# Performance work log

Measured on AMD Instinct MI355X. Metric: run time of the kernel, lower is better.

## Reference

```python
import jax, jax.numpy as jnp
import numpy as np

B, T, M, D, H, DH = 2, 2048, 2048, 384, 4, 96
NM, DF, R, NA = 8, 1536, 16, 4
S = 0.02  # weight init scale

PARAM_NAMES = ['cWq','cbq','cWk','cbk','cWv','cbv','cWo','cbo',
               'sWq','sbq','sWk','sbk','sWv','sbv','sWo','sbo',
               'gW','gb','f1W','f1b','f2W','f2b','adA','adB',
               'ln1g','ln1b','ln2g','ln2b','ln3g','ln3b']

def setup_inputs() -> dict:
    key = jax.random.key(0)
    ks = jax.random.split(key, 20)
    n = lambda k, sh, s=1.0: jax.random.normal(k, sh, dtype=jnp.float32) * s
    z = lambda sh: jnp.zeros(sh, dtype=jnp.float32)
    o = lambda sh: jnp.ones(sh, dtype=jnp.float32)
    return {
        'x': n(ks[0], (B, T, D)),
        'mem': n(ks[1], (B, M, D)),
        'motif_ctrl': n(ks[2], (B, NM)),
        'adapter_idx': 1,
        'cWq': n(ks[3], (D, D), S), 'cbq': z((D,)),
        'cWk': n(ks[4], (D, D), S), 'cbk': z((D,)),
        'cWv': n(ks[5], (D, D), S), 'cbv': z((D,)),
        'cWo': n(ks[6], (D, D), S), 'cbo': z((D,)),
        'sWq': n(ks[7], (D, D), S), 'sbq': z((D,)),
        'sWk': n(ks[8], (D, D), S), 'sbk': z((D,)),
        'sWv': n(ks[9], (D, D), S), 'sbv': z((D,)),
        'sWo': n(ks[10], (D, D), S), 'sbo': z((D,)),
        'gW': n(ks[11], (H, NM), S), 'gb': z((H,)),
        'f1W': n(ks[12], (DF, D), S), 'f1b': z((DF,)),
        'f2W': n(ks[13], (D, DF), S), 'f2b': z((D,)),
        'adA': n(ks[14], (NA, R, D), S),
        'adB': n(ks[15], (NA, D, R), S),
        'ln1g': o((D,)), 'ln1b': z((D,)),
        'ln2g': o((D,)), 'ln2b': z((D,)),
        'ln3g': o((D,)), 'ln3b': z((D,)),
    }

def _lin(x, W, b):
    return x @ W.T + b  # torch nn.Linear convention: W is [out, in]

def _layernorm(x, g, b):
    mu = x.mean(-1, keepdims=True)
    var = ((x - mu) ** 2).mean(-1, keepdims=True)
    return (x - mu) * jax.lax.rsqrt(var + 1e-5) * g + b

def _block(x, mem, motif_ctrl, adapter_idx, p):
    scale = 1.0 / np.sqrt(DH).astype(np.float32)
    # --- cross-attention over memory ---
    h = _layernorm(x, p['ln1g'], p['ln1b'])
    q = _lin(h, p['cWq'], p['cbq']).reshape(B, T, H, DH)
    k = _lin(mem, p['cWk'], p['cbk']).reshape(B, M, H, DH)
    v = _lin(mem, p['cWv'], p['cbv']).reshape(B, M, H, DH)
    A = jax.nn.softmax(jnp.einsum('bthd,bmhd->bhtm', q, k) * scale, axis=-1)
    z = jnp.einsum('bhtm,bmhd->bthd', A, v).reshape(B, T, D)
    x = x + _lin(z, p['cWo'], p['cbo'])
    # --- motif-gated self-attention (post-softmax per-head gate) ---
    h = _layernorm(x, p['ln2g'], p['ln2b'])
    gates = jax.nn.sigmoid(motif_ctrl @ p['gW'].T + p['gb'])  # [B, H]
    q = _lin(h, p['sWq'], p['sbq']).reshape(B, T, H, DH)
    k = _lin(h, p['sWk'], p['sbk']).reshape(B, T, H, DH)
    v = _lin(h, p['sWv'], p['sbv']).reshape(B, T, H, DH)
    A = jax.nn.softmax(jnp.einsum('bthd,bshd->bhts', q, k) * scale, axis=-1)
    A = A * gates[:, :, None, None]
    z = jnp.einsum('bhts,bshd->bthd', A, v).reshape(B, T, D)
    x = x + _lin(z, p['sWo'], p['sbo'])
    # --- LoRA-adapter FFN ---
    h = _layernorm(x, p['ln3g'], p['ln3b'])
    f = _lin(jax.nn.gelu(_lin(h, p['f1W'], p['f1b']), approximate=False), p['f2W'], p['f2b'])
    f = f + (h @ p['adA'][adapter_idx].T) @ p['adB'][adapter_idx].T
    return x + f

def reference(x, mem, motif_ctrl, adapter_idx,
              cWq, cbq, cWk, cbk, cWv, cbv, cWo, cbo,
              sWq, sbq, sWk, sbk, sWv, sbv, sWo, sbo,
              gW, gb, f1W, f1b, f2W, f2b, adA, adB,
              ln1g, ln1b, ln2g, ln2b, ln3g, ln3b):
    p = dict(zip(PARAM_NAMES, (cWq, cbq, cWk, cbk, cWv, cbv, cWo, cbo,
                               sWq, sbq, sWk, sbk, sWv, sbv, sWo, sbo,
                               gW, gb, f1W, f1b, f2W, f2b, adA, adB,
                               ln1g, ln1b, ln2g, ln2b, ln3g, ln3b)))
    return _block(x, mem, motif_ctrl, int(adapter_idx), p)
```

## Files before the change

### kernel.cpp

```cpp
#include <hip/hip_runtime.h>
#include <hip/hip_bf16.h>
#include <math.h>

#define B_   2
#define T_   2048
#define M_   2048
#define D_   384
#define H_   4
#define DH_  96
#define NM_  8
#define DF_  1536
#define R_   16
#define NR_  4096

typedef unsigned short u16;
typedef u16    u16x8  __attribute__((ext_vector_type(8)));
typedef u16    u16x4  __attribute__((ext_vector_type(4)));
typedef __bf16 bf16x8 __attribute__((ext_vector_type(8)));
typedef float  f32x4  __attribute__((ext_vector_type(4)));

union V8 { u16x8 u; bf16x8 b; };
__device__ __forceinline__ bf16x8 as_bf(u16x8 x) { V8 v; v.u = x; return v.b; }

__device__ __forceinline__ u16 f2bf(float f) {
    unsigned u = __float_as_uint(f);
    unsigned r = (u + 0x7fffu + ((u >> 16) & 1u)) >> 16;
    return (u16)r;
}
__device__ __forceinline__ float bf2f(u16 u) {
    return __uint_as_float(((unsigned)u) << 16);
}

__device__ __forceinline__ void load16(const u16* g, u16* l) {
    __builtin_amdgcn_global_load_lds(
        (const __attribute__((address_space(1))) void*)g,
        (__attribute__((address_space(3))) void*)l, 16, 0, 0);
}

__global__ __launch_bounds__(256)
void setup_kernel(const float* cWq, const float* cWk, const float* cWv, const float* cWo,
                  const float* sWq, const float* sWk, const float* sWv, const float* sWo,
                  const float* f1W, const float* f2W, const float* adA, const float* adB,
                  const float* mem,
                  u16* Wqkv_c, u16* Wco, u16* Wqkv_s, u16* Wso,
                  u16* Wf1, u16* Wf2, u16* WadA, u16* WadB, u16* memb,
                  const float* cbq, const float* cbk, const float* cbv,
                  const float* sbq, const float* sbk, const float* sbv,
                  float* bqkv_c, float* bqkv_s,
                  const float* mc, const float* gW, const float* gb, float* gates) {
    int seg = blockIdx.y;
    if (seg == 13) {
        for (int i = blockIdx.x * 256 + threadIdx.x; i < 2312; i += gridDim.x * 256) {
            if (i < 1152) {
                bqkv_c[i] = (i < 384) ? cbq[i] : (i < 768 ? cbk[i - 384] : cbv[i - 768]);
            } else if (i < 2304) {
                int j = i - 1152;
                bqkv_s[j] = (j < 384) ? sbq[j] : (j < 768 ? sbk[j - 384] : sbv[j - 768]);
            } else {
                int k = i - 2304;
                int b = k / H_, h = k % H_;
                float s = gb[h];
                for (int n = 0; n < NM_; n++)
                    s += mc[b * NM_ + n] * gW[h * NM_ + n];
                gates[k] = 1.f / (1.f + __expf(-s));
            }
        }
        return;
    }
    const float* s; u16* d; int n;
    switch (seg) {
        case 0:  s = cWq; d = Wqkv_c;           n = 147456; break;
        case 1:  s = cWk; d = Wqkv_c + 147456;  n = 147456; break;
        case 2:  s = cWv; d = Wqkv_c + 294912;  n = 147456; break;
        case 3:  s = cWo; d = Wco;              n = 147456; break;
        case 4:  s = sWq; d = Wqkv_s;           n = 147456; break;
        case 5:  s = sWk; d = Wqkv_s + 147456;  n = 147456; break;
        case 6:  s = sWv; d = Wqkv_s + 294912;  n = 147456; break;
        case 7:  s = sWo; d = Wso;              n = 147456; break;
        case 8:  s = f1W; d = Wf1;              n = 589824; break;
        case 9:  s = f2W; d = Wf2;              n = 589824; break;
        case 10: s = adA; d = WadA;             n = 24576;  break;
        case 11: s = adB; d = WadB;             n = 24576;  break;
        default: s = mem; d = memb;             n = 1572864; break;
    }
    for (int i = blockIdx.x * 256 + threadIdx.x; i < n; i += gridDim.x * 256)
        d[i] = f2bf(s[i]);
}

__global__ __launch_bounds__(384)
void ln_kernel(const float* __restrict__ x, const float* __restrict__ g,
               const float* __restrict__ b, u16* __restrict__ out) {
    __shared__ float sm[8];
    int row = blockIdx.x;
    int t = threadIdx.x;
    float v = x[(long)row * D_ + t];

    float s = v;
    for (int o = 32; o > 0; o >>= 1) s += __shfl_down(s, o);
    if ((t & 63) == 0) sm[t >> 6] = s;
    __syncthreads();
    float mu = 0.f;
    for (int i = 0; i < 6; i++) mu += sm[i];
    mu *= (1.f / D_);
    __syncthreads();

    float d = v - mu;
    s = d * d;
    for (int o = 32; o > 0; o >>= 1) s += __shfl_down(s, o);
    if ((t & 63) == 0) sm[t >> 6] = s;
    __syncthreads();
    float var = 0.f;
    for (int i = 0; i < 6; i++) var += sm[i];
    var *= (1.f / D_);

    float r = rsqrtf(var + 1e-5f);
    out[(long)row * D_ + t] = f2bf(d * r * g[t] + b[t]);
}

template<int MT, int ACT, bool OBF, bool VT, bool LORA, bool LORAA>
__global__ __launch_bounds__(256)
void gemm_uni(const u16* __restrict__ A0, const u16* __restrict__ A1, int aswitch,
              const u16* __restrict__ W, const float* __restrict__ bias,
              const float* __restrict__ res, void* __restrict__ Cout, int NC, int K,
              u16* __restrict__ Vt, int vtbase,
              const u16* __restrict__ Tl, const u16* __restrict__ adW,
              u16* __restrict__ TlOut, const int* __restrict__ aidx) {
    constexpr int NREG = 4 * MT + 8;
    constexpr int HALF = NREG * 512;
    __shared__ __align__(16) u16 S[2 * HALF];
    int tid = threadIdx.x, w = tid >> 6, lane = tid & 63;
    int l15 = lane & 15, quad = lane >> 4;
    int bm = blockIdx.y * (MT * 32), bn = blockIdx.x * 64;
    bool loraBlk = LORAA && (bn >= NC);

    const u16* Ap = (bn < aswitch) ? A0 : A1;
    const u16* Wb = W;
    if (LORAA && loraBlk) Wb = adW + (long)aidx[0] * 6144;

    const u16* GP[MT + 2];
    int LO[MT + 2];
    #pragma unroll
    for (int i = 0; i < MT + 2; i++) {
        int r = i * 4 + w;
        const u16* src;
        if (r < 4 * MT) {
            int mt = r >> 1, kc = r & 1;
            src = Ap + (long)(bm + mt * 16 + l15) * K + kc * 32 + quad * 8;
        } else {
            int rw = r - 4 * MT, nt = rw >> 1, kc = rw & 1;
            if (LORAA && loraBlk)
                src = Wb + (long)((nt * 16 + l15) & 15) * K + kc * 32 + quad * 8;
            else
                src = Wb + (long)(bn + nt * 16 + l15) * K + kc * 32 + quad * 8;
        }
        GP[i] = src;
        LO[i] = r * 512;
    }

    f32x4 acc[MT][2];
    #pragma unroll
    for (int s = 0; s < MT; s++)
        #pragma unroll
        for (int j = 0; j < 2; j++) acc[s][j] = (f32x4){0.f, 0.f, 0.f, 0.f};

    int niter = K >> 6;
    #pragma unroll
    for (int i = 0; i < MT + 2; i++) load16(GP[i], S + LO[i]);

    for (int it = 0; it < niter; it++) {
        __syncthreads();
        int cur = (it & 1) * HALF, nxt = HALF - cur;
        if (it + 1 < niter) {
            int k = (it + 1) << 6;
            #pragma unroll
            for (int i = 0; i < MT + 2; i++) load16(GP[i] + k, S + nxt + LO[i]);
        }
        #pragma unroll
        for (int kc = 0; kc < 2; kc++) {
            u16x8 af[MT], bfv[2];
            #pragma unroll
            for (int s = 0; s < MT; s++)
                af[s] = *(const u16x8*)(S + cur + (((w & 1) * MT + s) * 2 + kc) * 512 + lane * 8);
            #pragma unroll
            for (int j = 0; j < 2; j++)
                bfv[j] = *(const u16x8*)(S + cur + (4 * MT + (((w >> 1) * 2 + j) * 2 + kc)) * 512 + lane * 8);
            #pragma unroll
            for (int s = 0; s < MT; s++)
                #pragma unroll
                for (int j = 0; j < 2; j++)
                    acc[s][j] = __builtin_amdgcn_mfma_f32_16x16x32_bf16(
                        as_bf(af[s]), as_bf(bfv[j]), acc[s][j], 0, 0, 0);
        }
    }

    if (LORA) {
        long ao = (long)aidx[0] * 6144;
        u16x8 tlf[MT], adf[2];
        #pragma unroll
        for (int s = 0; s < MT; s++) {
            #pragma unroll
            for (int e = 0; e < 8; e++) tlf[s][e] = 0;
            if (quad < 2)
                tlf[s] = *(const u16x8*)(Tl + (long)(bm + ((w & 1) * MT + s) * 16 + l15) * 16 + quad * 8);
        }
        #pragma unroll
        for (int j = 0; j < 2; j++) {
            #pragma unroll
            for (int e = 0; e < 8; e++) adf[j][e] = 0;
            if (quad < 2)
                adf[j] = *(const u16x8*)(adW + ao + (long)(bn + ((w >> 1) * 2 + j) * 16 + l15) * 16 + quad * 8);
        }
        #pragma unroll
        for (int s = 0; s < MT; s++)
            #pragma unroll
            for (int j = 0; j < 2; j++)
                acc[s][j] = __builtin_amdgcn_mfma_f32_16x16x32_bf16(
                    as_bf(tlf[s]), as_bf(adf[j]), acc[s][j], 0, 0, 0);
    }

    #pragma unroll
    for (int mi = 0; mi < MT; mi++) {
        int mt = (w & 1) * MT + mi;
        int rowb = bm + mt * 16 + quad * 4;
        #pragma unroll
        for (int nj = 0; nj < 2; nj++) {
            int coll = ((w >> 1) * 2 + nj) * 16 + l15;
            int col = bn + coll;
            if (LORAA && loraBlk) {
                if (coll < 16) {
                    #pragma unroll
                    for (int r = 0; r < 4; r++)
                        TlOut[(long)(rowb + r) * 16 + coll] = f2bf(acc[mi][nj][r]);
                }
            } else {
                float bv = bias ? bias[col] : 0.f;
                if (VT && col >= vtbase) {
                    int vc = col - vtbase;
                    int b = rowb >> 11, rowl = rowb & 2047;
                    u16x4 ov;
                    #pragma unroll
                    for (int r = 0; r < 4; r++) ov[r] = f2bf(acc[mi][nj][r] + bv);
                    *(u16x4*)(Vt + ((long)b * 384 + vc) * 2048 + rowl) = ov;
                } else {
                    #pragma unroll
                    for (int r = 0; r < 4; r++) {
                        float v = acc[mi][nj][r] + bv;
                        if (ACT == 1) v = 0.5f * v * (1.f + erff(v * 0.70710678118654752f));
                        long idx = (long)(rowb + r) * NC + col;
                        if (res) v += res[idx];
                        if (OBF) ((u16*)Cout)[idx] = f2bf(v);
                        else     ((float*)Cout)[idx] = v;
                    }
                }
            }
        }
    }
}

__global__ __launch_bounds__(256)
void attn_mfma(const u16* __restrict__ Qg, int qs,
               const u16* __restrict__ Kg, int ks,
               const u16* __restrict__ Vt,
               u16* __restrict__ Po, float* __restrict__ Pl) {
    __shared__ __align__(16) u16 Ks[2][6144];
    __shared__ __align__(16) u16 Vs[2][6144];
    __shared__ __align__(16) u16 Ps[4][2][1088];
    const float SCALE = 0.10206207261596575f;

    int tid = threadIdx.x, wv = tid >> 6, lane = tid & 63;
    int l15 = lane & 15, quad = lane >> 4;
    int bh = blockIdx.y, b = bh >> 2, h = bh & 3;
    int split = blockIdx.z;
    int q0 = blockIdx.x * 128 + wv * 32;

    const u16* Qb = Qg + (long)(b * 2048 + q0) * qs + h * 96;
    const u16* Kb = Kg + (long)(b * 2048 + split * 512) * ks + h * 96;
    const u16* Vb = Vt + (long)(b * 384 + h * 96) * 2048 + split * 512;

    u16x8 qf[2][3];
    #pragma unroll
    for (int g = 0; g < 2; g++)
        #pragma unroll
        for (int t = 0; t < 3; t++)
            qf[g][t] = *(const u16x8*)(Qb + (long)(g * 16 + l15) * qs + t * 32 + quad * 8);

    f32x4 o[2][6];
    #pragma unroll
    for (int g = 0; g < 2; g++)
        #pragma unroll
        for (int i = 0; i < 6; i++) o[g][i] = (f32x4){0.f, 0.f, 0.f, 0.f};
    float rs[2][4] = {{0.f, 0.f, 0.f, 0.f}, {0.f, 0.f, 0.f, 0.f}};

    const u16* KgI[3]; int KlO[3]; const u16* VgI[3]; int VlO[3];
    #pragma unroll
    for (int i = 0; i < 3; i++) {
        int r = i * 4 + wv;
        int ksub = r & 3, kst = r >> 2;
        KgI[i] = Kb + (long)(ksub * 16 + l15) * ks + kst * 32 + quad * 8;
        KlO[i] = (ksub * 3 + kst) * 512;
        int nt = r >> 1, t2 = r & 1;
        VgI[i] = Vb + (long)(nt * 16 + l15) * 2048 + t2 * 32 + quad * 8;
        VlO[i] = r * 512;
    }

    #pragma unroll
    for (int i = 0; i < 3; i++) {
        load16(KgI[i], &Ks[0][0] + KlO[i]);
        load16(VgI[i], &Vs[0][0] + VlO[i]);
    }

    for (int it = 0; it < 8; it++) {
        __syncthreads();
        int cur = it & 1, nxt = cur ^ 1;
        if (it + 1 < 8) {
            int j = (it + 1) * 64;
            #pragma unroll
            for (int i = 0; i < 3; i++) {
                load16(KgI[i] + (long)j * ks, &Ks[nxt][0] + KlO[i]);
                load16(VgI[i] + j, &Vs[nxt][0] + VlO[i]);
            }
        }

        f32x4 sc[2][4];
        #pragma unroll
        for (int g = 0; g < 2; g++)
            #pragma unroll
            for (int s = 0; s < 4; s++) sc[g][s] = (f32x4){0.f, 0.f, 0.f, 0.f};
        #pragma unroll
        for (int s = 0; s < 4; s++)
            #pragma unroll
            for (int t = 0; t < 3; t++) {
                u16x8 kf = *(const u16x8*)(&Ks[cur][0] + (s * 3 + t) * 512 + lane * 8);
                sc[0][s] = __builtin_amdgcn_mfma_f32_16x16x32_bf16(as_bf(qf[0][t]), as_bf(kf), sc[0][s], 0, 0, 0);
                sc[1][s] = __builtin_amdgcn_mfma_f32_16x16x32_bf16(as_bf(qf[1][t]), as_bf(kf), sc[1][s], 0, 0, 0);
            }

        #pragma unroll
        for (int g = 0; g < 2; g++)
            #pragma unroll
            for (int s = 0; s < 4; s++) {
                int base = (s >> 1) * 544 + ((((s & 1) << 1) | (l15 >> 3))) * 136 + (l15 & 7);
                #pragma unroll
                for (int r = 0; r < 4; r++) {
                    float p = __expf(sc[g][s][r] * SCALE);
                    rs[g][r] += p;
                    Ps[wv][g][base + (quad * 4 + r) * 8] = f2bf(p);
                }
            }

        #pragma unroll
        for (int t2 = 0; t2 < 2; t2++) {
            u16x8 pf0 = *(const u16x8*)(&Ps[wv][0][0] + t2 * 544 + quad * 136 + l15 * 8);
            u16x8 pf1 = *(const u16x8*)(&Ps[wv][1][0] + t2 * 544 + quad * 136 + l15 * 8);
            #pragma unroll
            for (int nt = 0; nt < 6; nt++) {
                u16x8 vf = *(const u16x8*)(&Vs[cur][0] + (nt * 2 + t2) * 512 + lane * 8);
                o[0][nt] = __builtin_amdgcn_mfma_f32_16x16x32_bf16(as_bf(pf0), as_bf(vf), o[0][nt], 0, 0, 0);
                o[1][nt] = __builtin_amdgcn_mfma_f32_16x16x32_bf16(as_bf(pf1), as_bf(vf), o[1][nt], 0, 0, 0);
            }
        }
    }

    #pragma unroll
    for (int off = 1; off < 16; off <<= 1)
        #pragma unroll
        for (int g = 0; g < 2; g++)
            #pragma unroll
            for (int r = 0; r < 4; r++) rs[g][r] += __shfl_xor(rs[g][r], off);

    #pragma unroll
    for (int g = 0; g < 2; g++) {
        u16* Pob = Po + ((long)(split * 8 + bh) * 2048 + q0 + g * 16) * 96;
        #pragma unroll
        for (int nt = 0; nt < 6; nt++)
            #pragma unroll
            for (int r = 0; r < 4; r++)
                Pob[(long)(quad * 4 + r) * 96 + nt * 16 + l15] = f2bf(o[g][nt][r]);
        if (l15 == 0) {
            long mb = (long)(split * 8 + bh) * 2048 + q0 + g * 16 + quad * 4;
            #pragma unroll
            for (int r = 0; r < 4; r++) Pl[mb + r] = rs[g][r];
        }
    }
}

__global__ __launch_bounds__(256)
void attn_combine(const u16* __restrict__ Po, const float* __restrict__ Pl,
                  const float* __restrict__ gates, u16* __restrict__ Z) {
    int bh = blockIdx.y, b = bh >> 2, h = bh & 3;
    int tid = threadIdx.x;
    int rl = tid >> 2, part = tid & 3;
    int row = blockIdx.x * 64 + rl;
    long rbase = (long)bh * 2048 + row;

    float L = 0.f;
    #pragma unroll
    for (int s = 0; s < 4; s++) L += Pl[s * 16384 + rbase];
    float g = gates ? gates[bh] : 1.f;
    float sc = g / L;

    u16* Zr = Z + ((long)(b * 2048) + row) * 384 + h * 96 + part * 24;
    #pragma unroll
    for (int i = 0; i < 24; i += 4) {
        f32x4 acc = (f32x4){0.f, 0.f, 0.f, 0.f};
        #pragma unroll
        for (int s = 0; s < 4; s++) {
            u16x4 v = *(const u16x4*)(Po + ((long)s * 16384 + rbase) * 96 + part * 24 + i);
            #pragma unroll
            for (int e = 0; e < 4; e++) acc[e] += bf2f(v[e]);
        }
        u16x4 ov;
        #pragma unroll
        for (int e = 0; e < 4; e++) ov[e] = f2bf(acc[e] * sc);
        *(u16x4*)(Zr + i) = ov;
    }
}

extern "C" void kernel_launch(void* const* d_in, const int* in_sizes, int n_in,
                              void* d_out, int out_size, void* d_ws, size_t ws_size,
                              hipStream_t stream) {
    const float* x    = (const float*)d_in[0];
    const float* mem  = (const float*)d_in[1];
    const float* mc   = (const float*)d_in[2];
    const int*   aidx = (const int*)d_in[3];
    const float* cWq = (const float*)d_in[4],  *cbq = (const float*)d_in[5];
    const float* cWk = (const float*)d_in[6],  *cbk = (const float*)d_in[7];
    const float* cWv = (const float*)d_in[8],  *cbv = (const float*)d_in[9];
    const float* cWo = (const float*)d_in[10], *cbo = (const float*)d_in[11];
    const float* sWq = (const float*)d_in[12], *sbq = (const float*)d_in[13];
    const float* sWk = (const float*)d_in[14], *sbk = (const float*)d_in[15];
    const float* sWv = (const float*)d_in[16], *sbv = (const float*)d_in[17];
    const float* sWo = (const float*)d_in[18], *sbo = (const float*)d_in[19];
    const float* gW  = (const float*)d_in[20], *gb  = (const float*)d_in[21];
    const float* f1W = (const float*)d_in[22], *f1b = (const float*)d_in[23];
    const float* f2W = (const float*)d_in[24], *f2b = (const float*)d_in[25];
    const float* adA = (const float*)d_in[26], *adB = (const float*)d_in[27];
    const float* ln1g = (const float*)d_in[28], *ln1b = (const float*)d_in[29];
    const float* ln2g = (const float*)d_in[30], *ln2b = (const float*)d_in[31];
    const float* ln3g = (const float*)d_in[32], *ln3b = (const float*)d_in[33];

    u16* p = (u16*)d_ws;
    u16* H      = p; p += (size_t)NR_ * 384;
    u16* bufQKV = p; p += (size_t)NR_ * 1152;
    u16* Vt     = p; p += (size_t)B_ * 384 * 2048;
    u16* Zb     = p; p += (size_t)NR_ * 384;
    u16* F      = p; p += (size_t)NR_ * 1536;
    u16* Tl     = p; p += (size_t)NR_ * 16;
    u16* memb   = p; p += (size_t)NR_ * 384;
    u16* Wqkv_c = p; p += 442368;
    u16* Wco    = p; p += 147456;
    u16* Wqkv_s = p; p += 442368;
    u16* Wso    = p; p += 147456;
    u16* Wf1    = p; p += 589824;
    u16* Wf2    = p; p += 589824;
    u16* WadA   = p; p += 24576;
    u16* WadB   = p; p += 24576;
    u16* Po     = p; p += (size_t)4 * 8 * 2048 * 96;
    p += ((size_t)p & 1);
    float* fp = (float*)(((size_t)p + 3) & ~(size_t)3);
    float* X1 = fp;     fp += (size_t)NR_ * 384;
    float* X2 = fp;     fp += (size_t)NR_ * 384;
    float* Pl = fp;     fp += (size_t)4 * 8 * 2048;
    float* bqkv_c = fp; fp += 1152;
    float* bqkv_s = fp; fp += 1152;
    float* gbuf   = fp; fp += 8;

    setup_kernel<<<dim3(96, 14), 256, 0, stream>>>(
        cWq, cWk, cWv, cWo, sWq, sWk, sWv, sWo, f1W, f2W, adA, adB, mem,
        Wqkv_c, Wco, Wqkv_s, Wso, Wf1, Wf2, WadA, WadB, memb,
        cbq, cbk, cbv, sbq, sbk, sbv, bqkv_c, bqkv_s, mc, gW, gb, gbuf);

    const float* nf = nullptr;
    const u16* nu = nullptr;
    ln_kernel<<<NR_, 384, 0, stream>>>(x, ln1g, ln1b, H);
    gemm_uni<2, 0, true, true, false, false><<<dim3(18, 64), 256, 0, stream>>>(
        H, memb, 384, Wqkv_c, bqkv_c, nf, bufQKV, 1152, 384, Vt, 768, nu, nu, nullptr, nullptr);
    attn_mfma<<<dim3(16, 8, 4), 256, 0, stream>>>(bufQKV, 1152, bufQKV + 384, 1152, Vt, Po, Pl);
    attn_combine<<<dim3(32, 8), 256, 0, stream>>>(Po, Pl, nullptr, Zb);
    gemm_uni<1, 0, false, false, false, false><<<dim3(6, 128), 256, 0, stream>>>(
        Zb, Zb, 0, Wco, cbo, x, X1, 384, 384, nullptr, 0, nu, nu, nullptr, nullptr);

    ln_kernel<<<NR_, 384, 0, stream>>>(X1, ln2g, ln2b, H);
    gemm_uni<2, 0, true, true, false, false><<<dim3(18, 64), 256, 0, stream>>>(
        H, H, 0, Wqkv_s, bqkv_s, nf, bufQKV, 1152, 384, Vt, 768, nu, nu, nullptr, nullptr);
    attn_mfma<<<dim3(16, 8, 4), 256, 0, stream>>>(bufQKV, 1152, bufQKV + 384, 1152, Vt, Po, Pl);
    attn_combine<<<dim3(32, 8), 256, 0, stream>>>(Po, Pl, gbuf, Zb);
    gemm_uni<1, 0, false, false, false, false><<<dim3(6, 128), 256, 0, stream>>>(
        Zb, Zb, 0, Wso, sbo, X1, X2, 384, 384, nullptr, 0, nu, nu, nullptr, nullptr);

    ln_kernel<<<NR_, 384, 0, stream>>>(X2, ln3g, ln3b, H);
    gemm_uni<2, 1, true, false, false, true><<<dim3(25, 64), 256, 0, stream>>>(
        H, H, 0, Wf1, f1b, nf, F, 1536, 384, nullptr, 0, nu, WadA, Tl, aidx);
    gemm_uni<1, 0, false, false, true, false><<<dim3(6, 128), 256, 0, stream>>>(
        F, F, 0, Wf2, f2b, X2, d_out, 384, 1536, nullptr, 0, Tl, WadB, nullptr, aidx);
}
```

Baseline: 355.1 us.

## Double attention KV split count and shrink LDS footprint with single-buffered V

Raises the key-dimension split of the attention kernel from 4 to 8, so each block covers 256 keys in 4 iterations and the grid doubles to 1024 blocks. V is now single-buffered and loaded in the same iteration it is consumed, with an extra barrier before the PV MFMAs. The P scratch padding is removed. This cuts LDS use, which may allow more resident blocks and better occupancy. In exchange, the V load is no longer overlapped with compute, the combine kernel reads twice as many partials, and the unpadded P layout may cause LDS bank conflicts.

```diff
diff --git a/kernel.cpp b/kernel.cpp
--- a/kernel.cpp
+++ b/kernel.cpp
@@ -12,6 +12,7 @@
 #define DF_  1536
 #define R_   16
 #define NR_  4096
+#define SPL  8
 
 typedef unsigned short u16;
 typedef u16    u16x8  __attribute__((ext_vector_type(8)));
@@ -263,8 +264,8 @@
                const u16* __restrict__ Vt,
                u16* __restrict__ Po, float* __restrict__ Pl) {
     __shared__ __align__(16) u16 Ks[2][6144];
-    __shared__ __align__(16) u16 Vs[2][6144];
-    __shared__ __align__(16) u16 Ps[4][2][1088];
+    __shared__ __align__(16) u16 Vs[6144];
+    __shared__ __align__(16) u16 Ps[4][2][1024];
     const float SCALE = 0.10206207261596575f;
 
     int tid = threadIdx.x, wv = tid >> 6, lane = tid & 63;
@@ -274,8 +275,8 @@
     int q0 = blockIdx.x * 128 + wv * 32;
 
     const u16* Qb = Qg + (long)(b * 2048 + q0) * qs + h * 96;
-    const u16* Kb = Kg + (long)(b * 2048 + split * 512) * ks + h * 96;
-    const u16* Vb = Vt + (long)(b * 384 + h * 96) * 2048 + split * 512;
+    const u16* Kb = Kg + (long)(b * 2048 + split * 256) * ks + h * 96;
+    const u16* Vb = Vt + (long)(b * 384 + h * 96) * 2048 + split * 256;
 
     u16x8 qf[2][3];
     #pragma unroll
@@ -291,7 +292,7 @@
         for (int i = 0; i < 6; i++) o[g][i] = (f32x4){0.f, 0.f, 0.f, 0.f};
     float rs[2][4] = {{0.f, 0.f, 0.f, 0.f}, {0.f, 0.f, 0.f, 0.f}};
 
-    const u16* KgI[3]; int KlO[3]; const u16* VgI[3]; int VlO[3];
+    const u16* KgI[3]; int KlO[3]; const u16* VgI[3]; u16* VlP[3];
     #pragma unroll
     for (int i = 0; i < 3; i++) {
         int r = i * 4 + wv;
@@ -300,25 +301,22 @@
         KlO[i] = (ksub * 3 + kst) * 512;
         int nt = r >> 1, t2 = r & 1;
         VgI[i] = Vb + (long)(nt * 16 + l15) * 2048 + t2 * 32 + quad * 8;
-        VlO[i] = r * 512;
-    }
-
-    #pragma unroll
-    for (int i = 0; i < 3; i++) {
-        load16(KgI[i], &Ks[0][0] + KlO[i]);
-        load16(VgI[i], &Vs[0][0] + VlO[i]);
-    }
-
-    for (int it = 0; it < 8; it++) {
+        VlP[i] = &Vs[0] + r * 512;
+    }
+
+    #pragma unroll
+    for (int i = 0; i < 3; i++) load16(KgI[i], &Ks[0][0] + KlO[i]);
+
+    for (int it = 0; it < 4; it++) {
+        int cur = it & 1, nxt = cur ^ 1;
         __syncthreads();
-        int cur = it & 1, nxt = cur ^ 1;
-        if (it + 1 < 8) {
-            int j = (it + 1) * 64;
-            #pragma unroll
-            for (int i = 0; i < 3; i++) {
-                load16(KgI[i] + (long)j * ks, &Ks[nxt][0] + KlO[i]);
-                load16(VgI[i] + j, &Vs[nxt][0] + VlO[i]);
-            }
+        int j = it * 64;
+        #pragma unroll
+        for (int i = 0; i < 3; i++) load16(VgI[i] + j, VlP[i]);
+        if (it + 1 < 4) {
+            int jn = (it + 1) * 64;
+            #pragma unroll
+            for (int i = 0; i < 3; i++) load16(KgI[i] + (long)jn * ks, &Ks[nxt][0] + KlO[i]);
         }
 
         f32x4 sc[2][4];
@@ -339,7 +337,7 @@
         for (int g = 0; g < 2; g++)
             #pragma unroll
             for (int s = 0; s < 4; s++) {
-                int base = (s >> 1) * 544 + ((((s & 1) << 1) | (l15 >> 3))) * 136 + (l15 & 7);
+                int base = (s >> 1) * 512 + ((((s & 1) << 1) | (l15 >> 3))) * 128 + (l15 & 7);
                 #pragma unroll
                 for (int r = 0; r < 4; r++) {
                     float p = __expf(sc[g][s][r] * SCALE);
@@ -348,13 +346,14 @@
                 }
             }
 
+        __syncthreads();
         #pragma unroll
         for (int t2 = 0; t2 < 2; t2++) {
-            u16x8 pf0 = *(const u16x8*)(&Ps[wv][0][0] + t2 * 544 + quad * 136 + l15 * 8);
-            u16x8 pf1 = *(const u16x8*)(&Ps[wv][1][0] + t2 * 544 + quad * 136 + l15 * 8);
+            u16x8 pf0 = *(const u16x8*)(&Ps[wv][0][0] + t2 * 512 + quad * 128 + l15 * 8);
+            u16x8 pf1 = *(const u16x8*)(&Ps[wv][1][0] + t2 * 512 + quad * 128 + l15 * 8);
             #pragma unroll
             for (int nt = 0; nt < 6; nt++) {
-                u16x8 vf = *(const u16x8*)(&Vs[cur][0] + (nt * 2 + t2) * 512 + lane * 8);
+                u16x8 vf = *(const u16x8*)(&Vs[0] + (nt * 2 + t2) * 512 + lane * 8);
                 o[0][nt] = __builtin_amdgcn_mfma_f32_16x16x32_bf16(as_bf(pf0), as_bf(vf), o[0][nt], 0, 0, 0);
                 o[1][nt] = __builtin_amdgcn_mfma_f32_16x16x32_bf16(as_bf(pf1), as_bf(vf), o[1][nt], 0, 0, 0);
             }
@@ -395,7 +394,7 @@
 
     float L = 0.f;
     #pragma unroll
-    for (int s = 0; s < 4; s++) L += Pl[s * 16384 + rbase];
+    for (int s = 0; s < SPL; s++) L += Pl[s * 16384 + rbase];
     float g = gates ? gates[bh] : 1.f;
     float sc = g / L;
 
@@ -404,7 +403,7 @@
     for (int i = 0; i < 24; i += 4) {
         f32x4 acc = (f32x4){0.f, 0.f, 0.f, 0.f};
         #pragma unroll
-        for (int s = 0; s < 4; s++) {
+        for (int s = 0; s < SPL; s++) {
             u16x4 v = *(const u16x4*)(Po + ((long)s * 16384 + rbase) * 96 + part * 24 + i);
             #pragma unroll
             for (int e = 0; e < 4; e++) acc[e] += bf2f(v[e]);
@@ -455,12 +454,11 @@
     u16* Wf2    = p; p += 589824;
     u16* WadA   = p; p += 24576;
     u16* WadB   = p; p += 24576;
-    u16* Po     = p; p += (size_t)4 * 8 * 2048 * 96;
-    p += ((size_t)p & 1);
+    u16* Po     = p; p += (size_t)SPL * 8 * 2048 * 96;
     float* fp = (float*)(((size_t)p + 3) & ~(size_t)3);
     float* X1 = fp;     fp += (size_t)NR_ * 384;
     float* X2 = fp;     fp += (size_t)NR_ * 384;
-    float* Pl = fp;     fp += (size_t)4 * 8 * 2048;
+    float* Pl = fp;     fp += (size_t)SPL * 8 * 2048;
     float* bqkv_c = fp; fp += 1152;
     float* bqkv_s = fp; fp += 1152;
     float* gbuf   = fp; fp += 8;
@@ -475,7 +473,7 @@
     ln_kernel<<<NR_, 384, 0, stream>>>(x, ln1g, ln1b, H);
     gemm_uni<2, 0, true, true, false, false><<<dim3(18, 64), 256, 0, stream>>>(
         H, memb, 384, Wqkv_c, bqkv_c, nf, bufQKV, 1152, 384, Vt, 768, nu, nu, nullptr, nullptr);
-    attn_mfma<<<dim3(16, 8, 4), 256, 0, stream>>>(bufQKV, 1152, bufQKV + 384, 1152, Vt, Po, Pl);
+    attn_mfma<<<dim3(16, 8, SPL), 256, 0, stream>>>(bufQKV, 1152, bufQKV + 384, 1152, Vt, Po, Pl);
     attn_combine<<<dim3(32, 8), 256, 0, stream>>>(Po, Pl, nullptr, Zb);
     gemm_uni<1, 0, false, false, false, false><<<dim3(6, 128), 256, 0, stream>>>(
         Zb, Zb, 0, Wco, cbo, x, X1, 384, 384, nullptr, 0, nu, nu, nullptr, nullptr);
@@ -483,7 +481,7 @@
     ln_kernel<<<NR_, 384, 0, stream>>>(X1, ln2g, ln2b, H);
     gemm_uni<2, 0, true, true, false, false><<<dim3(18, 64), 256, 0, stream>>>(
         H, H, 0, Wqkv_s, bqkv_s, nf, bufQKV, 1152, 384, Vt, 768, nu, nu, nullptr, nullptr);
-    attn_mfma<<<dim3(16, 8, 4), 256, 0, stream>>>(bufQKV, 1152, bufQKV + 384, 1152, Vt, Po, Pl);
+    attn_mfma<<<dim3(16, 8, SPL), 256, 0, stream>>>(bufQKV, 1152, bufQKV + 384, 1152, Vt, Po, Pl);
     attn_combine<<<dim3(32, 8), 256, 0, stream>>>(Po, Pl, gbuf, Zb);
     gemm_uni<1, 0, false, false, false, false><<<dim3(6, 128), 256, 0, stream>>>(
         Zb, Zb, 0, Wso, sbo, X1, X2, 384, 384, nullptr, 0, nu, nu, nullptr, nullptr);
```

After: 363.4 us. 1.02x slower.

## Fuse LayerNorm into QKV/FFN GEMM prologue and attention combine into output-projection GEMM

Applied to the files above, without the earlier changes.

Removes the standalone LayerNorm and attention-combine kernels. LayerNorm statistics are now computed per 64-row tile inside the following GEMM, which normalizes fp32 rows to bf16 while staging the A tile into shared memory. The split-K attention partials are summed and scaled inside the output-projection GEMM prologue. This saves launches and the intermediate H/Z round trips through global memory, at the cost of recomputing LN statistics in every N-block, register-path A loads instead of async copies, and a one-pass variance formula.

```diff
diff --git a/kernel.cpp b/kernel.cpp
--- a/kernel.cpp
+++ b/kernel.cpp
@@ -12,6 +12,7 @@
 #define DF_  1536
 #define R_   16
 #define NR_  4096
+#define SPL  4
 
 typedef unsigned short u16;
 typedef u16    u16x8  __attribute__((ext_vector_type(8)));
@@ -87,105 +88,129 @@
         d[i] = f2bf(s[i]);
 }
 
-__global__ __launch_bounds__(384)
-void ln_kernel(const float* __restrict__ x, const float* __restrict__ g,
-               const float* __restrict__ b, u16* __restrict__ out) {
-    __shared__ float sm[8];
-    int row = blockIdx.x;
-    int t = threadIdx.x;
-    float v = x[(long)row * D_ + t];
-
-    float s = v;
-    for (int o = 32; o > 0; o >>= 1) s += __shfl_down(s, o);
-    if ((t & 63) == 0) sm[t >> 6] = s;
-    __syncthreads();
-    float mu = 0.f;
-    for (int i = 0; i < 6; i++) mu += sm[i];
-    mu *= (1.f / D_);
-    __syncthreads();
-
-    float d = v - mu;
-    s = d * d;
-    for (int o = 32; o > 0; o >>= 1) s += __shfl_down(s, o);
-    if ((t & 63) == 0) sm[t >> 6] = s;
-    __syncthreads();
-    float var = 0.f;
-    for (int i = 0; i < 6; i++) var += sm[i];
-    var *= (1.f / D_);
-
-    float r = rsqrtf(var + 1e-5f);
-    out[(long)row * D_ + t] = f2bf(d * r * g[t] + b[t]);
-}
-
-template<int MT, int ACT, bool OBF, bool VT, bool LORA, bool LORAA>
+template<int ACT, bool OBF, bool VT, bool LORAA>
 __global__ __launch_bounds__(256)
-void gemm_uni(const u16* __restrict__ A0, const u16* __restrict__ A1, int aswitch,
-              const u16* __restrict__ W, const float* __restrict__ bias,
-              const float* __restrict__ res, void* __restrict__ Cout, int NC, int K,
-              u16* __restrict__ Vt, int vtbase,
-              const u16* __restrict__ Tl, const u16* __restrict__ adW,
-              u16* __restrict__ TlOut, const int* __restrict__ aidx) {
-    constexpr int NREG = 4 * MT + 8;
-    constexpr int HALF = NREG * 512;
-    __shared__ __align__(16) u16 S[2 * HALF];
+void gemm_ln(const float* __restrict__ Xf, const u16* __restrict__ A1, int aswitch,
+             const float* __restrict__ lng, const float* __restrict__ lnb,
+             const u16* __restrict__ W, const float* __restrict__ bias,
+             void* __restrict__ Cout, int NC,
+             u16* __restrict__ Vt, int vtbase,
+             const u16* __restrict__ adW, u16* __restrict__ TlOut,
+             const int* __restrict__ aidx) {
+    const int K = 384;
+    __shared__ __align__(16) u16 SA[2][4096];
+    __shared__ __align__(16) u16 SW[2][4096];
+    __shared__ float smu[64], sr[64];
+    __shared__ float slg[384], slb[384];
     int tid = threadIdx.x, w = tid >> 6, lane = tid & 63;
     int l15 = lane & 15, quad = lane >> 4;
-    int bm = blockIdx.y * (MT * 32), bn = blockIdx.x * 64;
+    int bm = blockIdx.y * 64, bn = blockIdx.x * 64;
     bool loraBlk = LORAA && (bn >= NC);
-
-    const u16* Ap = (bn < aswitch) ? A0 : A1;
+    bool pass = (bn >= aswitch);
+
     const u16* Wb = W;
     if (LORAA && loraBlk) Wb = adW + (long)aidx[0] * 6144;
 
-    const u16* GP[MT + 2];
-    int LO[MT + 2];
-    #pragma unroll
-    for (int i = 0; i < MT + 2; i++) {
-        int r = i * 4 + w;
-        const u16* src;
-        if (r < 4 * MT) {
-            int mt = r >> 1, kc = r & 1;
-            src = Ap + (long)(bm + mt * 16 + l15) * K + kc * 32 + quad * 8;
-        } else {
-            int rw = r - 4 * MT, nt = rw >> 1, kc = rw & 1;
-            if (LORAA && loraBlk)
-                src = Wb + (long)((nt * 16 + l15) & 15) * K + kc * 32 + quad * 8;
-            else
-                src = Wb + (long)(bn + nt * 16 + l15) * K + kc * 32 + quad * 8;
-        }
-        GP[i] = src;
-        LO[i] = r * 512;
-    }
-
-    f32x4 acc[MT][2];
-    #pragma unroll
-    for (int s = 0; s < MT; s++)
+    const u16* WG[2]; int WO[2];
+    #pragma unroll
+    for (int i = 0; i < 2; i++) {
+        int r = i * 4 + w, nt = r >> 1, kc = r & 1;
+        int wrow = (LORAA && loraBlk) ? ((nt * 16 + l15) & 15) : (bn + nt * 16 + l15);
+        WG[i] = Wb + (long)wrow * K + kc * 32 + quad * 8;
+        WO[i] = r * 512;
+    }
+
+    if (!pass) {
+        int row = tid >> 2, q4 = tid & 3;
+        const float* src = Xf + (long)(bm + row) * K + q4 * 96;
+        float s = 0.f, s2 = 0.f;
+        #pragma unroll
+        for (int i = 0; i < 24; i++) {
+            f32x4 v = *(const f32x4*)(src + i * 4);
+            #pragma unroll
+            for (int e = 0; e < 4; e++) { s += v[e]; s2 += v[e] * v[e]; }
+        }
+        s  += __shfl_xor(s, 1);  s  += __shfl_xor(s, 2);
+        s2 += __shfl_xor(s2, 1); s2 += __shfl_xor(s2, 2);
+        if (q4 == 0) {
+            float mu = s * (1.f / 384.f);
+            float var = s2 * (1.f / 384.f) - mu * mu;
+            smu[row] = mu;
+            sr[row] = rsqrtf(var + 1e-5f);
+        }
+        if (tid < 192) {
+            f32x4 g4 = *(const f32x4*)(lng + tid * 2);
+            slg[tid * 2] = g4[0]; slg[tid * 2 + 1] = g4[1];
+            f32x4 b4 = *(const f32x4*)(lnb + tid * 2);
+            slb[tid * 2] = b4[0]; slb[tid * 2 + 1] = b4[1];
+        }
+    }
+    #pragma unroll
+    for (int i = 0; i < 2; i++) load16(WG[i], &SW[0][0] + WO[i]);
+    __syncthreads();
+
+    {
+        int row = tid & 63;
+        #pragma unroll
+        for (int i = 0; i < 2; i++) {
+            int kg = (tid >> 6) + i * 4;
+            int k = kg * 8;
+            u16x8 hv;
+            if (pass) {
+                hv = *(const u16x8*)(A1 + (long)(bm + row) * K + k);
+            } else {
+                const float* src = Xf + (long)(bm + row) * K + k;
+                float mu = smu[row], r = sr[row];
+                #pragma unroll
+                for (int e = 0; e < 8; e++)
+                    hv[e] = f2bf((src[e] - mu) * r * slg[k + e] + slb[k + e]);
+            }
+            *(u16x8*)(&SA[0][0] + ((row >> 4) * 2 + (kg >> 2)) * 512 + (kg & 3) * 128 + (row & 15) * 8) = hv;
+        }
+    }
+
+    f32x4 acc[2][2];
+    #pragma unroll
+    for (int s = 0; s < 2; s++)
         #pragma unroll
         for (int j = 0; j < 2; j++) acc[s][j] = (f32x4){0.f, 0.f, 0.f, 0.f};
 
-    int niter = K >> 6;
-    #pragma unroll
-    for (int i = 0; i < MT + 2; i++) load16(GP[i], S + LO[i]);
-
-    for (int it = 0; it < niter; it++) {
+    for (int it = 0; it < 6; it++) {
         __syncthreads();
-        int cur = (it & 1) * HALF, nxt = HALF - cur;
-        if (it + 1 < niter) {
-            int k = (it + 1) << 6;
-            #pragma unroll
-            for (int i = 0; i < MT + 2; i++) load16(GP[i] + k, S + nxt + LO[i]);
+        int cur = it & 1, nxt = cur ^ 1;
+        if (it + 1 < 6) {
+            int k0 = (it + 1) * 64;
+            #pragma unroll
+            for (int i = 0; i < 2; i++) load16(WG[i] + k0, &SW[nxt][0] + WO[i]);
+            int row = tid & 63;
+            #pragma unroll
+            for (int i = 0; i < 2; i++) {
+                int kg = (tid >> 6) + i * 4;
+                int k = k0 + kg * 8;
+                u16x8 hv;
+                if (pass) {
+                    hv = *(const u16x8*)(A1 + (long)(bm + row) * K + k);
+                } else {
+                    const float* src = Xf + (long)(bm + row) * K + k;
+                    float mu = smu[row], r = sr[row];
+                    #pragma unroll
+                    for (int e = 0; e < 8; e++)
+                        hv[e] = f2bf((src[e] - mu) * r * slg[k + e] + slb[k + e]);
+                }
+                *(u16x8*)(&SA[nxt][0] + ((row >> 4) * 2 + (kg >> 2)) * 512 + (kg & 3) * 128 + (row & 15) * 8) = hv;
+            }
         }
         #pragma unroll
         for (int kc = 0; kc < 2; kc++) {
-            u16x8 af[MT], bfv[2];
-            #pragma unroll
-            for (int s = 0; s < MT; s++)
-                af[s] = *(const u16x8*)(S + cur + (((w & 1) * MT + s) * 2 + kc) * 512 + lane * 8);
+            u16x8 af[2], bfv[2];
+            #pragma unroll
+            for (int s = 0; s < 2; s++)
+                af[s] = *(const u16x8*)(&SA[cur][0] + (((w & 1) * 2 + s) * 2 + kc) * 512 + lane * 8);
             #pragma unroll
             for (int j = 0; j < 2; j++)
-                bfv[j] = *(const u16x8*)(S + cur + (4 * MT + (((w >> 1) * 2 + j) * 2 + kc)) * 512 + lane * 8);
-            #pragma unroll
-            for (int s = 0; s < MT; s++)
+                bfv[j] = *(const u16x8*)(&SW[cur][0] + ((((w >> 1) * 2 + j)) * 2 + kc) * 512 + lane * 8);
+            #pragma unroll
+            for (int s = 0; s < 2; s++)
                 #pragma unroll
                 for (int j = 0; j < 2; j++)
                     acc[s][j] = __builtin_amdgcn_mfma_f32_16x16x32_bf16(
@@ -193,35 +218,9 @@
         }
     }
 
-    if (LORA) {
-        long ao = (long)aidx[0] * 6144;
-        u16x8 tlf[MT], adf[2];
-        #pragma unroll
-        for (int s = 0; s < MT; s++) {
-            #pragma unroll
-            for (int e = 0; e < 8; e++) tlf[s][e] = 0;
-            if (quad < 2)
-                tlf[s] = *(const u16x8*)(Tl + (long)(bm + ((w & 1) * MT + s) * 16 + l15) * 16 + quad * 8);
-        }
-        #pragma unroll
-        for (int j = 0; j < 2; j++) {
-            #pragma unroll
-            for (int e = 0; e < 8; e++) adf[j][e] = 0;
-            if (quad < 2)
-                adf[j] = *(const u16x8*)(adW + ao + (long)(bn + ((w >> 1) * 2 + j) * 16 + l15) * 16 + quad * 8);
-        }
-        #pragma unroll
-        for (int s = 0; s < MT; s++)
-            #pragma unroll
-            for (int j = 0; j < 2; j++)
-                acc[s][j] = __builtin_amdgcn_mfma_f32_16x16x32_bf16(
-                    as_bf(tlf[s]), as_bf(adf[j]), acc[s][j], 0, 0, 0);
-    }
-
-    #pragma unroll
-    for (int mi = 0; mi < MT; mi++) {
-        int mt = (w & 1) * MT + mi;
-        int rowb = bm + mt * 16 + quad * 4;
+    #pragma unroll
+    for (int mi = 0; mi < 2; mi++) {
+        int rowb = bm + ((w & 1) * 2 + mi) * 16 + quad * 4;
         #pragma unroll
         for (int nj = 0; nj < 2; nj++) {
             int coll = ((w >> 1) * 2 + nj) * 16 + l15;
@@ -246,13 +245,205 @@
                     for (int r = 0; r < 4; r++) {
                         float v = acc[mi][nj][r] + bv;
                         if (ACT == 1) v = 0.5f * v * (1.f + erff(v * 0.70710678118654752f));
-                        long idx = (long)(rowb + r) * NC + col;
-                        if (res) v += res[idx];
-                        if (OBF) ((u16*)Cout)[idx] = f2bf(v);
-                        else     ((float*)Cout)[idx] = v;
+                        ((u16*)Cout)[(long)(rowb + r) * NC + col] = f2bf(v);
                     }
                 }
             }
+        }
+    }
+}
+
+__global__ __launch_bounds__(256)
+void gemm_comb(const u16* __restrict__ Po, const float* __restrict__ Pl,
+               const float* __restrict__ gates,
+               const u16* __restrict__ W, const float* __restrict__ bias,
+               const float* __restrict__ res, float* __restrict__ Cout) {
+    const int K = 384, NC = 384;
+    __shared__ __align__(16) u16 SA[2][2048];
+    __shared__ __align__(16) u16 SW[2][4096];
+    __shared__ float ssc[32][4];
+    int tid = threadIdx.x, w = tid >> 6, lane = tid & 63;
+    int l15 = lane & 15, quad = lane >> 4;
+    int bm = blockIdx.y * 32, bn = blockIdx.x * 64;
+
+    const u16* WG[2]; int WO[2];
+    #pragma unroll
+    for (int i = 0; i < 2; i++) {
+        int r = i * 4 + w, nt = r >> 1, kc = r & 1;
+        WG[i] = W + (long)(bn + nt * 16 + l15) * K + kc * 32 + quad * 8;
+        WO[i] = r * 512;
+    }
+
+    if (tid < 128) {
+        int row = tid >> 2, h = tid & 3;
+        int grow = bm + row, b = grow >> 11, tl = grow & 2047;
+        float L = 0.f;
+        #pragma unroll
+        for (int s = 0; s < SPL; s++) L += Pl[(long)(s * 8 + b * 4 + h) * 2048 + tl];
+        float g = gates ? gates[b * 4 + h] : 1.f;
+        ssc[row][h] = g / L;
+    }
+    #pragma unroll
+    for (int i = 0; i < 2; i++) load16(WG[i], &SW[0][0] + WO[i]);
+    __syncthreads();
+
+    int row = tid & 31, kg = tid >> 5;
+    int grow = bm + row, b = grow >> 11, tl = grow & 2047;
+    {
+        int k = kg * 8;
+        int h = k / 96, d = k - h * 96;
+        const u16* base = Po + ((long)(b * 4 + h) * 2048 + tl) * 96 + d;
+        float a[8] = {0.f, 0.f, 0.f, 0.f, 0.f, 0.f, 0.f, 0.f};
+        #pragma unroll
+        for (int s = 0; s < SPL; s++) {
+            u16x8 v = *(const u16x8*)(base + (long)s * 1572864);
+            #pragma unroll
+            for (int e = 0; e < 8; e++) a[e] += bf2f(v[e]);
+        }
+        float sc = ssc[row][h];
+        u16x8 hv;
+        #pragma unroll
+        for (int e = 0; e < 8; e++) hv[e] = f2bf(a[e] * sc);
+        *(u16x8*)(&SA[0][0] + ((row >> 4) * 2 + (kg >> 2)) * 512 + (kg & 3) * 128 + (row & 15) * 8) = hv;
+    }
+
+    f32x4 acc[2];
+    acc[0] = (f32x4){0.f, 0.f, 0.f, 0.f};
+    acc[1] = (f32x4){0.f, 0.f, 0.f, 0.f};
+
+    for (int it = 0; it < 6; it++) {
+        __syncthreads();
+        int cur = it & 1, nxt = cur ^ 1;
+        if (it + 1 < 6) {
+            int k0 = (it + 1) * 64;
+            #pragma unroll
+            for (int i = 0; i < 2; i++) load16(WG[i] + k0, &SW[nxt][0] + WO[i]);
+            int k = k0 + kg * 8;
+            int h = k / 96, d = k - h * 96;
+            const u16* base = Po + ((long)(b * 4 + h) * 2048 + tl) * 96 + d;
+            float a[8] = {0.f, 0.f, 0.f, 0.f, 0.f, 0.f, 0.f, 0.f};
+            #pragma unroll
+            for (int s = 0; s < SPL; s++) {
+                u16x8 v = *(const u16x8*)(base + (long)s * 1572864);
+                #pragma unroll
+                for (int e = 0; e < 8; e++) a[e] += bf2f(v[e]);
+            }
+            float sc = ssc[row][h];
+            u16x8 hv;
+            #pragma unroll
+            for (int e = 0; e < 8; e++) hv[e] = f2bf(a[e] * sc);
+            *(u16x8*)(&SA[nxt][0] + ((row >> 4) * 2 + (kg >> 2)) * 512 + (kg & 3) * 128 + (row & 15) * 8) = hv;
+        }
+        #pragma unroll
+        for (int kc = 0; kc < 2; kc++) {
+            u16x8 af, bfv[2];
+            af = *(const u16x8*)(&SA[cur][0] + ((w & 1) * 2 + kc) * 512 + lane * 8);
+            #pragma unroll
+            for (int j = 0; j < 2; j++)
+                bfv[j] = *(const u16x8*)(&SW[cur][0] + (((w >> 1) * 2 + j) * 2 + kc) * 512 + lane * 8);
+            #pragma unroll
+            for (int j = 0; j < 2; j++)
+                acc[j] = __builtin_amdgcn_mfma_f32_16x16x32_bf16(
+                    as_bf(af), as_bf(bfv[j]), acc[j], 0, 0, 0);
+        }
+    }
+
+    int rowb = bm + (w & 1) * 16 + quad * 4;
+    #pragma unroll
+    for (int nj = 0; nj < 2; nj++) {
+        int col = bn + ((w >> 1) * 2 + nj) * 16 + l15;
+        float bv = bias[col];
+        #pragma unroll
+        for (int r = 0; r < 4; r++) {
+            long idx = (long)(rowb + r) * NC + col;
+            Cout[idx] = acc[nj][r] + bv + res[idx];
+        }
+    }
+}
+
+__global__ __launch_bounds__(256)
+void gemm_f2(const u16* __restrict__ A, const u16* __restrict__ W,
+             const float* __restrict__ bias, const float* __restrict__ res,
+             float* __restrict__ Cout, int NC, int K,
+             const u16* __restrict__ Tl, const u16* __restrict__ adW,
+             const int* __restrict__ aidx) {
+    constexpr int HALF = 12 * 512;
+    __shared__ __align__(16) u16 S[2 * HALF];
+    int tid = threadIdx.x, w = tid >> 6, lane = tid & 63;
+    int l15 = lane & 15, quad = lane >> 4;
+    int bm = blockIdx.y * 32, bn = blockIdx.x * 64;
+
+    const u16* GP[3]; int LO[3];
+    #pragma unroll
+    for (int i = 0; i < 3; i++) {
+        int r = i * 4 + w;
+        const u16* src;
+        if (r < 4) {
+            int mt = r >> 1, kc = r & 1;
+            src = A + (long)(bm + mt * 16 + l15) * K + kc * 32 + quad * 8;
+        } else {
+            int rw = r - 4, nt = rw >> 1, kc = rw & 1;
+            src = W + (long)(bn + nt * 16 + l15) * K + kc * 32 + quad * 8;
+        }
+        GP[i] = src;
+        LO[i] = r * 512;
+    }
+
+    f32x4 acc[2];
+    acc[0] = (f32x4){0.f, 0.f, 0.f, 0.f};
+    acc[1] = (f32x4){0.f, 0.f, 0.f, 0.f};
+
+    int niter = K >> 6;
+    #pragma unroll
+    for (int i = 0; i < 3; i++) load16(GP[i], S + LO[i]);
+
+    for (int it = 0; it < niter; it++) {
+        __syncthreads();
+        int cur = (it & 1) * HALF, nxt = HALF - cur;
+        if (it + 1 < niter) {
+            int k = (it + 1) << 6;
+            #pragma unroll
+            for (int i = 0; i < 3; i++) load16(GP[i] + k, S + nxt + LO[i]);
+        }
+        #pragma unroll
+        for (int kc = 0; kc < 2; kc++) {
+            u16x8 af, bfv[2];
+            af = *(const u16x8*)(S + cur + ((w & 1) * 2 + kc) * 512 + lane * 8);
+            #pragma unroll
+            for (int j = 0; j < 2; j++)
+                bfv[j] = *(const u16x8*)(S + cur + (4 + ((w >> 1) * 2 + j) * 2 + kc) * 512 + lane * 8);
+            #pragma unroll
+            for (int j = 0; j < 2; j++)
+                acc[j] = __builtin_amdgcn_mfma_f32_16x16x32_bf16(
+                    as_bf(af), as_bf(bfv[j]), acc[j], 0, 0, 0);
+        }
+    }
+
+    {
+        long ao = (long)aidx[0] * 6144;
+        u16x8 tlf = {0, 0, 0, 0, 0, 0, 0, 0};
+        u16x8 adf[2] = {{0, 0, 0, 0, 0, 0, 0, 0}, {0, 0, 0, 0, 0, 0, 0, 0}};
+        if (quad < 2) {
+            tlf = *(const u16x8*)(Tl + (long)(bm + (w & 1) * 16 + l15) * 16 + quad * 8);
+            #pragma unroll
+            for (int j = 0; j < 2; j++)
+                adf[j] = *(const u16x8*)(adW + ao + (long)(bn + ((w >> 1) * 2 + j) * 16 + l15) * 16 + quad * 8);
+        }
+        #pragma unroll
+        for (int j = 0; j < 2; j++)
+            acc[j] = __builtin_amdgcn_mfma_f32_16x16x32_bf16(
+                as_bf(tlf), as_bf(adf[j]), acc[j], 0, 0, 0);
+    }
+
+    int rowb = bm + (w & 1) * 16 + quad * 4;
+    #pragma unroll
+    for (int nj = 0; nj < 2; nj++) {
+        int col = bn + ((w >> 1) * 2 + nj) * 16 + l15;
+        float bv = bias[col];
+        #pragma unroll
+        for (int r = 0; r < 4; r++) {
+            long idx = (long)(rowb + r) * NC + col;
+            Cout[idx] = acc[nj][r] + bv + res[idx];
         }
     }
 }
@@ -381,38 +572,6 @@
             #pragma unroll
             for (int r = 0; r < 4; r++) Pl[mb + r] = rs[g][r];
         }
-    }
-}
-
-__global__ __launch_bounds__(256)
-void attn_combine(const u16* __restrict__ Po, const float* __restrict__ Pl,
-                  const float* __restrict__ gates, u16* __restrict__ Z) {
-    int bh = blockIdx.y, b = bh >> 2, h = bh & 3;
-    int tid = threadIdx.x;
-    int rl = tid >> 2, part = tid & 3;
-    int row = blockIdx.x * 64 + rl;
-    long rbase = (long)bh * 2048 + row;
-
-    float L = 0.f;
-    #pragma unroll
-    for (int s = 0; s < 4; s++) L += Pl[s * 16384 + rbase];
-    float g = gates ? gates[bh] : 1.f;
-    float sc = g / L;
-
-    u16* Zr = Z + ((long)(b * 2048) + row) * 384 + h * 96 + part * 24;
-    #pragma unroll
-    for (int i = 0; i < 24; i += 4) {
-        f32x4 acc = (f32x4){0.f, 0.f, 0.f, 0.f};
-        #pragma unroll
-        for (int s = 0; s < 4; s++) {
-            u16x4 v = *(const u16x4*)(Po + ((long)s * 16384 + rbase) * 96 + part * 24 + i);
-            #pragma unroll
-            for (int e = 0; e < 4; e++) acc[e] += bf2f(v[e]);
-        }
-        u16x4 ov;
-        #pragma unroll
-        for (int e = 0; e < 4; e++) ov[e] = f2bf(acc[e] * sc);
-        *(u16x4*)(Zr + i) = ov;
     }
 }
 
@@ -440,10 +599,8 @@
     const float* ln3g = (const float*)d_in[32], *ln3b = (const float*)d_in[33];
 
     u16* p = (u16*)d_ws;
-    u16* H      = p; p += (size_t)NR_ * 384;
     u16* bufQKV = p; p += (size_t)NR_ * 1152;
     u16* Vt     = p; p += (size_t)B_ * 384 * 2048;
-    u16* Zb     = p; p += (size_t)NR_ * 384;
     u16* F      = p; p += (size_t)NR_ * 1536;
     u16* Tl     = p; p += (size_t)NR_ * 16;
     u16* memb   = p; p += (size_t)NR_ * 384;
@@ -455,12 +612,11 @@
     u16* Wf2    = p; p += 589824;
     u16* WadA   = p; p += 24576;
     u16* WadB   = p; p += 24576;
-    u16* Po     = p; p += (size_t)4 * 8 * 2048 * 96;
-    p += ((size_t)p & 1);
+    u16* Po     = p; p += (size_t)SPL * 8 * 2048 * 96;
     float* fp = (float*)(((size_t)p + 3) & ~(size_t)3);
     float* X1 = fp;     fp += (size_t)NR_ * 384;
     float* X2 = fp;     fp += (size_t)NR_ * 384;
-    float* Pl = fp;     fp += (size_t)4 * 8 * 2048;
+    float* Pl = fp;     fp += (size_t)SPL * 8 * 2048;
     float* bqkv_c = fp; fp += 1152;
     float* bqkv_s = fp; fp += 1152;
     float* gbuf   = fp; fp += 8;
@@ -470,27 +626,18 @@
         Wqkv_c, Wco, Wqkv_s, Wso, Wf1, Wf2, WadA, WadB, memb,
         cbq, cbk, cbv, sbq, sbk, sbv, bqkv_c, bqkv_s, mc, gW, gb, gbuf);
 
-    const float* nf = nullptr;
-    const u16* nu = nullptr;
-    ln_kernel<<<NR_, 384, 0, stream>>>(x, ln1g, ln1b, H);
-    gemm_uni<2, 0, true, true, false, false><<<dim3(18, 64), 256, 0, stream>>>(
-        H, memb, 384, Wqkv_c, bqkv_c, nf, bufQKV, 1152, 384, Vt, 768, nu, nu, nullptr, nullptr);
-    attn_mfma<<<dim3(16, 8, 4), 256, 0, stream>>>(bufQKV, 1152, bufQKV + 384, 1152, Vt, Po, Pl);
-    attn_combine<<<dim3(32, 8), 256, 0, stream>>>(Po, Pl, nullptr, Zb);
-    gemm_uni<1, 0, false, false, false, false><<<dim3(6, 128), 256, 0, stream>>>(
-        Zb, Zb, 0, Wco, cbo, x, X1, 384, 384, nullptr, 0, nu, nu, nullptr, nullptr);
-
-    ln_kernel<<<NR_, 384, 0, stream>>>(X1, ln2g, ln2b, H);
-    gemm_uni<2, 0, true, true, false, false><<<dim3(18, 64), 256, 0, stream>>>(
-        H, H, 0, Wqkv_s, bqkv_s, nf, bufQKV, 1152, 384, Vt, 768, nu, nu, nullptr, nullptr);
-    attn_mfma<<<dim3(16, 8, 4), 256, 0, stream>>>(bufQKV, 1152, bufQKV + 384, 1152, Vt, Po, Pl);
-    attn_combine<<<dim3(32, 8), 256, 0, stream>>>(Po, Pl, gbuf, Zb);
-    gemm_uni<1, 0, false, false, false, false><<<dim3(6, 128), 256, 0, stream>>>(
-        Zb, Zb, 0, Wso, sbo, X1, X2, 384, 384, nullptr, 0, nu, nu, nullptr, nullptr);
-
-    ln_kernel<<<NR_, 384, 0, stream>>>(X2, ln3g, ln3b, H);
-    gemm_uni<2, 1, true, false, false, true><<<dim3(25, 64), 256, 0, stream>>>(
-        H, H, 0, Wf1, f1b, nf, F, 1536, 384, nullptr, 0, nu, WadA, Tl, aidx);
-    gemm_uni<1, 0, false, false, true, false><<<dim3(6, 128), 256, 0, stream>>>(
-        F, F, 0, Wf2, f2b, X2, d_out, 384, 1536, nullptr, 0, Tl, WadB, nullptr, aidx);
-}
+    gemm_ln<0, true, true, false><<<dim3(18, 64), 256, 0, stream>>>(
+        x, memb, 384, ln1g, ln1b, Wqkv_c, bqkv_c, bufQKV, 1152, Vt, 768, nullptr, nullptr, nullptr);
+    attn_mfma<<<dim3(16, 8, SPL), 256, 0, stream>>>(bufQKV, 1152, bufQKV + 384, 1152, Vt, Po, Pl);
+    gemm_comb<<<dim3(6, 128), 256, 0, stream>>>(Po, Pl, nullptr, Wco, cbo, x, X1);
+
+    gemm_ln<0, true, true, false><<<dim3(18, 64), 256, 0, stream>>>(
+        X1, nullptr, 1 << 30, ln2g, ln2b, Wqkv_s, bqkv_s, bufQKV, 1152, Vt, 768, nullptr, nullptr, nullptr);
+    attn_mfma<<<dim3(16, 8, SPL), 256, 0, stream>>>(bufQKV, 1152, bufQKV + 384, 1152, Vt, Po, Pl);
+    gemm_comb<<<dim3(6, 128), 256, 0, stream>>>(Po, Pl, gbuf, Wso, sbo, X1, X2);
+
+    gemm_ln<1, true, false, true><<<dim3(25, 64), 256, 0, stream>>>(
+        X2, nullptr, 1 << 30, ln3g, ln3b, Wf1, f1b, F, 1536, nullptr, 0, WadA, Tl, aidx);
+    gemm_f2<<<dim3(6, 128), 256, 0, stream>>>(
+        F, Wf2, f2b, X2, (float*)d_out, 384, 1536, Tl, WadB, aidx);
+}
```

After: 393.2 us. 10.7% more time.
